# Performance work log

Measured on AMD Instinct MI355X. Metric: run time of the kernel, lower is better.

The kernel has to match this reference:

```python
import jax, jax.numpy as jnp
import numpy as np
from jax import lax

K = 2000      # node_num of GraphConvolution
H, W = 75, 100  # edge_region_feature spatial grid (from per-pixel concat loops)


def setup_inputs() -> dict:
    key = jax.random.key(0)
    k1, k2, k3, k4 = jax.random.split(key, 4)
    b, c = 8, 512
    edge_region_feature = jax.random.normal(k1, (b, c, H, W), dtype=jnp.float32)
    edge_region_predict = jax.random.normal(k2, (b, 3, H, W), dtype=jnp.float32)
    # GraphConvolution params: kaiming_normal_(fan_out) weights, zero bias
    w1 = jax.random.normal(k3, (512, 128), dtype=jnp.float32) * np.sqrt(2.0 / 128)
    b1 = jnp.zeros((K, 128), dtype=jnp.float32)
    w2 = jax.random.normal(k4, (128, 128), dtype=jnp.float32) * np.sqrt(2.0 / 128)
    b2 = jnp.zeros((K, 128), dtype=jnp.float32)
    return {"edge_region_feature": edge_region_feature,
            "edge_region_predict": edge_region_predict,
            "w1": w1, "b1": b1, "w2": w2, "b2": b2}


def reference(edge_region_feature, edge_region_predict, w1, b1, w2, b2):
    b, c = edge_region_feature.shape[0], edge_region_feature.shape[1]
    # block_feature built as: for x in range(W) for y in range(H) -> node n at (y=n%H, x=n//H)
    block = jnp.transpose(edge_region_feature, (0, 3, 2, 1)).reshape(b, W * H, c)  # (b, 7500, 512)

    # topk over channel-0 prediction, flattened row-major (idx = y*W + x)
    scores = edge_region_predict[:, 0, :, :].reshape(b, -1)            # (b, 7500)
    _vals, topk_idx = lax.top_k(scores, K)
    sorted_idx = jnp.sort(topk_idx, axis=1)                            # (b, 2000) int32

    # gather node features (replicates original's indexing of block_feature)
    node_map = jnp.take_along_axis(block, sorted_idx[:, :, None], axis=1)  # (b, 2000, 512)

    # generate_adjacent_map: decode positions with width=W, connect 8-neighborhood (+self)
    py = sorted_idx // W
    px = sorted_idx % W
    near_y = jnp.abs(py[:, :, None] - py[:, None, :]) <= 1
    near_x = jnp.abs(px[:, :, None] - px[:, None, :]) <= 1
    adj = (near_y & near_x).astype(jnp.float32)                        # (b, 2000, 2000)

    # node_feature_grouping = ReLU6 -> GCN(512->128) -> GCN(128->128)
    inp = jnp.clip(jnp.concatenate([adj, node_map], axis=2), 0.0, 6.0)  # ReLU6 on cat(adj, nodes)
    a = inp[:, :, :K]
    nf = inp[:, :, K:]
    # GCN1: A @ X @ W1 + b1  (in!=out -> no residual)
    x1 = jnp.einsum('bij,bjf->bif', a, nf) @ w1 + b1                   # (b, 2000, 128)
    # GCN2: A @ X1 @ W2 + b2 + X1 (in==out -> residual)
    x2 = jnp.einsum('bij,bjf->bif', a, x1) @ w2 + b2 + x1              # (b, 2000, 128)

    node_output_feature = jnp.tanh(x2)
    return node_output_feature, sorted_idx
```

## Files before the change

kernel.cpp:

```cpp
#include <hip/hip_runtime.h>
#include <cmath>

#define H_DIM 75
#define W_DIM 100
#define HW 7500
#define KSEL 2000
#define BATCH 8
#define CIN 512
#define FDIM 128

typedef short v4s __attribute__((ext_vector_type(4)));
typedef short v8s __attribute__((ext_vector_type(8)));
typedef float v16f __attribute__((ext_vector_type(16)));

__device__ __forceinline__ unsigned int map_key(float f) {
  unsigned int u = __float_as_uint(f);
  return (u & 0x80000000u) ? ~u : (u | 0x80000000u);
}

__device__ __forceinline__ float fast_tanh(float x) {
  float e = __expf(2.0f * x);
  return 1.0f - 2.0f * __builtin_amdgcn_rcpf(e + 1.0f);
}

__device__ __forceinline__ unsigned short bf16_rne(float v) {
  unsigned int u = __float_as_uint(v);
  unsigned int r = u + 0x7FFFu + ((u >> 16) & 1u);
  return (unsigned short)(r >> 16);
}
__device__ __forceinline__ float bf16_to_f(unsigned short h) {
  return __uint_as_float(((unsigned int)h) << 16);
}

__global__ __launch_bounds__(1024) void topk_nbr_kernel(
    const float* __restrict__ pred, const float* __restrict__ w1,
    const float* __restrict__ w2,
    int* __restrict__ off_ws, float* __restrict__ out_idx,
    unsigned short* __restrict__ nbr, unsigned char* __restrict__ cnt,
    unsigned short* __restrict__ w1t_hi, unsigned short* __restrict__ w1t_lo,
    unsigned short* __restrict__ w2t_hi, unsigned short* __restrict__ w2t_lo)
{
  __shared__ unsigned int keys[HW];
  __shared__ unsigned int whist[16 * 256];
  __shared__ unsigned int hist[256];
  __shared__ unsigned int partials[16];
  __shared__ unsigned int s_prefix, s_kth;
  const int tid = threadIdx.x;

  if (blockIdx.x >= BATCH) {
    int base = (blockIdx.x - BATCH) * 1024 + tid;
    for (int e = base; e < CIN * FDIM + FDIM * FDIM; e += 8 * 1024) {
      if (e < CIN * FDIM) {
        int k = e & (CIN - 1), f = e >> 9;
        float v = w1[k * FDIM + f];
        unsigned short hi = bf16_rne(v);
        unsigned short lo = bf16_rne(v - bf16_to_f(hi));
        w1t_hi[(size_t)f * CIN + k] = hi;
        w1t_lo[(size_t)f * CIN + k] = lo;
      } else {
        int e2 = e - CIN * FDIM;
        int k = e2 & (FDIM - 1), f = e2 >> 7;
        float v = w2[k * FDIM + f];
        unsigned short hi = bf16_rne(v);
        unsigned short lo = bf16_rne(v - bf16_to_f(hi));
        w2t_hi[(size_t)f * FDIM + k] = hi;
        w2t_lo[(size_t)f * FDIM + k] = lo;
      }
    }
    return;
  }

  const int b = blockIdx.x;
  const int lane = tid & 63, w = tid >> 6;
  const float* scores = pred + (size_t)b * 3 * HW;
  for (int i = tid; i < HW; i += 1024) keys[i] = map_key(scores[i]);
  if (tid == 0) { s_prefix = 0u; s_kth = KSEL; }
  __syncthreads();

  for (int shift = 24; shift >= 0; shift -= 8) {
    for (int i = tid; i < 16 * 256; i += 1024) whist[i] = 0u;
    __syncthreads();
    unsigned int pref = s_prefix;
    unsigned int maskhi = (shift == 24) ? 0u : (0xFFFFFFFFu << (shift + 8));
    for (int i = tid; i < HW; i += 1024) {
      unsigned int k = keys[i];
      if ((k & maskhi) == pref)
        atomicAdd(&whist[w * 256 + ((k >> shift) & 0xFFu)], 1u);
    }
    __syncthreads();
    if (tid < 256) {
      unsigned int s = 0;
      #pragma unroll
      for (int ww = 0; ww < 16; ++ww) s += whist[ww * 256 + tid];
      hist[tid] = s;
    }
    __syncthreads();
    if (tid < 64) {
      unsigned int b0 = hist[tid * 4], b1 = hist[tid * 4 + 1];
      unsigned int b2 = hist[tid * 4 + 2], b3 = hist[tid * 4 + 3];
      unsigned int kth = s_kth;
      unsigned int T = b0 + b1 + b2 + b3;
      #pragma unroll
      for (int off = 1; off < 64; off <<= 1) {
        unsigned int t = __shfl_down(T, off, 64);
        if (tid + off < 64) T += t;
      }
      unsigned int U = __shfl_down(T, 1, 64);
      if (tid == 63) U = 0u;
      unsigned int s3 = b3 + U, s2 = b2 + s3, s1 = b1 + s2, s0 = b0 + s1;
      if (s0 >= kth && s1 < kth) { s_prefix = pref | ((unsigned)(4 * tid + 0) << shift); s_kth = kth - s1; }
      if (s1 >= kth && s2 < kth) { s_prefix = pref | ((unsigned)(4 * tid + 1) << shift); s_kth = kth - s2; }
      if (s2 >= kth && s3 < kth) { s_prefix = pref | ((unsigned)(4 * tid + 2) << shift); s_kth = kth - s3; }
      if (s3 >= kth && U  < kth) { s_prefix = pref | ((unsigned)(4 * tid + 3) << shift); s_kth = kth - U; }
    }
    __syncthreads();
  }
  const unsigned int thresh = s_prefix;

  unsigned int local[8];
  unsigned int sum = 0;
  #pragma unroll
  for (int e = 0; e < 8; ++e) {
    int i = tid * 8 + e;
    unsigned int p = 0;
    if (i < HW) {
      unsigned int ky = keys[i];
      if (ky > thresh) p = 1u;
      else if (ky == thresh) p = (1u << 16);
    }
    local[e] = p; sum += p;
  }
  __syncthreads();
  short* pos_of  = (short*)keys;
  int*   s_idx_sh = (int*)((char*)keys + 15000);
  for (int i = tid; i < HW; i += 1024) pos_of[i] = -1;

  unsigned int inc = sum;
  #pragma unroll
  for (int off = 1; off < 64; off <<= 1) {
    unsigned int t = __shfl_up(inc, off, 64);
    if (lane >= off) inc += t;
  }
  if (lane == 63) partials[w] = inc;
  __syncthreads();
  if (tid < 16) {
    unsigned int v = partials[tid];
    #pragma unroll
    for (int off = 1; off < 16; off <<= 1) {
      unsigned int t = __shfl_up(v, off, 64);
      if (tid >= off) v += t;
    }
    partials[tid] = v;
  }
  __syncthreads();
  unsigned int total = partials[15];
  unsigned int run = (w ? partials[w - 1] : 0u) + inc - sum;
  unsigned int ties = (unsigned int)KSEL - (total & 0xFFFFu);
  #pragma unroll
  for (int e = 0; e < 8; ++e) {
    int i = tid * 8 + e;
    unsigned int p = local[e];
    unsigned int gt_pref = run & 0xFFFFu;
    unsigned int eq_pref = run >> 16;
    bool sel = (p & 1u) || (((p >> 16) != 0u) && eq_pref < ties);
    if (sel) {
      unsigned int pos = gt_pref + (eq_pref < ties ? eq_pref : ties);
      off_ws[b * KSEL + pos] = (i % H_DIM) * W_DIM + i / H_DIM;
      out_idx[b * KSEL + pos] = (float)i;
      s_idx_sh[pos] = i;
      pos_of[i] = (short)pos;
    }
    run += p;
  }
  __syncthreads();

  for (int i = tid; i < KSEL; i += 1024) {
    int q = s_idx_sh[i];
    int py = q / W_DIM, px = q % W_DIM;
    unsigned short tmp[9];
    int c = 0;
    #pragma unroll
    for (int dy = -1; dy <= 1; ++dy) {
      int y = py + dy;
      if ((unsigned)y >= (unsigned)H_DIM) continue;
      #pragma unroll
      for (int dx = -1; dx <= 1; ++dx) {
        int x = px + dx;
        if ((unsigned)x >= (unsigned)W_DIM) continue;
        short p = pos_of[y * W_DIM + x];
        if (p >= 0) tmp[c++] = (unsigned short)p;
      }
    }
    #pragma unroll
    for (int t = 0; t < 9; ++t)
      nbr[(size_t)(b * KSEL + i) * 9 + t] = (t < c) ? tmp[t] : (unsigned short)0;
    cnt[b * KSEL + i] = (unsigned char)c;
  }
}

__global__ __launch_bounds__(256) void gemm1_fused(
    const float* __restrict__ feat, const int* __restrict__ off_ws,
    const unsigned short* __restrict__ w1t_hi,
    const unsigned short* __restrict__ w1t_lo,
    float* __restrict__ G)
{
  __shared__ unsigned short a_hi[2][64][20], a_lo[2][64][20];
  const int b = blockIdx.y;
  const int n0 = blockIdx.x * 64;
  const int tid = threadIdx.x;
  const int lane = tid & 63, w = tid >> 6;
  const int wr = w & 1, wc = w >> 1;
  const int q = lane >> 5, m = lane & 31;
  v16f acc0, acc1;
  #pragma unroll
  for (int i = 0; i < 16; ++i) { acc0[i] = 0.f; acc1[i] = 0.f; }
  const int an = wr * 32 + m;
  const int f0 = wc * 64 + m;
  const int n_st = tid & 63, ks = (tid >> 6) * 4;
  int nidx = n0 + n_st;
  if (nidx > KSEL - 1) nidx = KSEL - 1;
  const float* fb = feat + (size_t)b * CIN * HW + off_ws[b * KSEL + nidx];

  #pragma unroll
  for (int j = 0; j < 4; ++j) {
    float v = fb[(size_t)(ks + j) * HW];
    v = fminf(fmaxf(v, 0.f), 6.f);
    unsigned short hi = bf16_rne(v);
    a_hi[0][n_st][ks + j] = hi;
    a_lo[0][n_st][ks + j] = bf16_rne(v - bf16_to_f(hi));
  }
  __syncthreads();

  for (int k0 = 0; k0 < CIN; k0 += 16) {
    const int p = (k0 >> 4) & 1;
    if (k0 + 16 < CIN) {
      #pragma unroll
      for (int j = 0; j < 4; ++j) {
        float v = fb[(size_t)(k0 + 16 + ks + j) * HW];
        v = fminf(fmaxf(v, 0.f), 6.f);
        unsigned short hi = bf16_rne(v);
        a_hi[p ^ 1][n_st][ks + j] = hi;
        a_lo[p ^ 1][n_st][ks + j] = bf16_rne(v - bf16_to_f(hi));
      }
    }
    v4s ah0 = *(const v4s*)&a_hi[p][an][q * 8];
    v4s ah1 = *(const v4s*)&a_hi[p][an][q * 8 + 4];
    v4s al0 = *(const v4s*)&a_lo[p][an][q * 8];
    v4s al1 = *(const v4s*)&a_lo[p][an][q * 8 + 4];
    v8s avh = __builtin_shufflevector(ah0, ah1, 0, 1, 2, 3, 4, 5, 6, 7);
    v8s avl = __builtin_shufflevector(al0, al1, 0, 1, 2, 3, 4, 5, 6, 7);
    v8s b0h = *(const v8s*)&w1t_hi[(size_t)f0 * CIN + k0 + q * 8];
    v8s b0l = *(const v8s*)&w1t_lo[(size_t)f0 * CIN + k0 + q * 8];
    v8s b1h = *(const v8s*)&w1t_hi[(size_t)(f0 + 32) * CIN + k0 + q * 8];
    v8s b1l = *(const v8s*)&w1t_lo[(size_t)(f0 + 32) * CIN + k0 + q * 8];
    acc0 = __builtin_amdgcn_mfma_f32_32x32x16_bf16(avh, b0h, acc0, 0, 0, 0);
    acc0 = __builtin_amdgcn_mfma_f32_32x32x16_bf16(avh, b0l, acc0, 0, 0, 0);
    acc0 = __builtin_amdgcn_mfma_f32_32x32x16_bf16(avl, b0h, acc0, 0, 0, 0);
    acc1 = __builtin_amdgcn_mfma_f32_32x32x16_bf16(avh, b1h, acc1, 0, 0, 0);
    acc1 = __builtin_amdgcn_mfma_f32_32x32x16_bf16(avh, b1l, acc1, 0, 0, 0);
    acc1 = __builtin_amdgcn_mfma_f32_32x32x16_bf16(avl, b1h, acc1, 0, 0, 0);
    __syncthreads();
  }
  float* ob = G + (size_t)b * KSEL * FDIM;
  #pragma unroll
  for (int reg = 0; reg < 16; ++reg) {
    int row = n0 + wr * 32 + (reg & 3) + 8 * (reg >> 2) + 4 * q;
    if (row < KSEL) {
      ob[(size_t)row * FDIM + f0]      = acc0[reg];
      ob[(size_t)row * FDIM + f0 + 32] = acc1[reg];
    }
  }
}

__global__ __launch_bounds__(256) void gemm2_fused(
    const float* __restrict__ G, const float* __restrict__ b1,
    const unsigned short* __restrict__ nbr, const unsigned char* __restrict__ cnt,
    const unsigned short* __restrict__ w2t_hi,
    const unsigned short* __restrict__ w2t_lo,
    float* __restrict__ x1, float* __restrict__ Hm)
{
  __shared__ __align__(16) unsigned short xh[64][FDIM];
  __shared__ __align__(16) unsigned short xl[64][FDIM];
  const int b = blockIdx.y;
  const int n0 = blockIdx.x * 64;
  const int tid = threadIdx.x;
  const int g = tid >> 5, lane32 = tid & 31;
  const float4* G4 = (const float4*)G + (size_t)b * KSEL * 32;

  #pragma unroll 2
  for (int rr = 0; rr < 8; ++rr) {
    const int r = rr * 8 + g;
    const int node = n0 + r;
    const int nodec = (node > KSEL - 1) ? KSEL - 1 : node;
    const size_t bi = (size_t)b * KSEL + nodec;
    const unsigned short* nb = nbr + bi * 9;
    unsigned short idx[9];
    #pragma unroll
    for (int t = 0; t < 9; ++t) idx[t] = nb[t];
    const int c = cnt[bi];
    float4 v[9];
    #pragma unroll
    for (int t = 0; t < 9; ++t) v[t] = G4[(size_t)idx[t] * 32 + lane32];
    float4 acc = ((const float4*)b1)[nodec * 32 + lane32];
    #pragma unroll
    for (int t = 0; t < 9; ++t) {
      float mk = (t < c) ? 1.f : 0.f;
      acc.x = fmaf(v[t].x, mk, acc.x);
      acc.y = fmaf(v[t].y, mk, acc.y);
      acc.z = fmaf(v[t].z, mk, acc.z);
      acc.w = fmaf(v[t].w, mk, acc.w);
    }
    if (node < KSEL) ((float4*)x1)[bi * 32 + lane32] = acc;
    ushort4 h, l;
    h.x = bf16_rne(acc.x); l.x = bf16_rne(acc.x - bf16_to_f(h.x));
    h.y = bf16_rne(acc.y); l.y = bf16_rne(acc.y - bf16_to_f(h.y));
    h.z = bf16_rne(acc.z); l.z = bf16_rne(acc.z - bf16_to_f(h.z));
    h.w = bf16_rne(acc.w); l.w = bf16_rne(acc.w - bf16_to_f(h.w));
    const int cs = (lane32 * 4) ^ ((r & 15) << 3);
    *(ushort4*)&xh[r][cs] = h;
    *(ushort4*)&xl[r][cs] = l;
  }
  __syncthreads();

  const int lane = tid & 63, w = tid >> 6;
  const int wr = w & 1, wc = w >> 1;
  const int q = lane >> 5, m = lane & 31;
  const int ar = wr * 32 + m;
  const int f0 = wc * 64 + m;
  v16f acc0, acc1;
  #pragma unroll
  for (int i = 0; i < 16; ++i) { acc0[i] = 0.f; acc1[i] = 0.f; }
  #pragma unroll
  for (int k0 = 0; k0 < FDIM; k0 += 16) {
    const int ac = (k0 + q * 8) ^ ((ar & 15) << 3);
    v8s avh = *(const v8s*)&xh[ar][ac];
    v8s avl = *(const v8s*)&xl[ar][ac];
    v8s b0h = *(const v8s*)&w2t_hi[(size_t)f0 * FDIM + k0 + q * 8];
    v8s b0l = *(const v8s*)&w2t_lo[(size_t)f0 * FDIM + k0 + q * 8];
    v8s b1h = *(const v8s*)&w2t_hi[(size_t)(f0 + 32) * FDIM + k0 + q * 8];
    v8s b1l = *(const v8s*)&w2t_lo[(size_t)(f0 + 32) * FDIM + k0 + q * 8];
    acc0 = __builtin_amdgcn_mfma_f32_32x32x16_bf16(avh, b0h, acc0, 0, 0, 0);
    acc0 = __builtin_amdgcn_mfma_f32_32x32x16_bf16(avh, b0l, acc0, 0, 0, 0);
    acc0 = __builtin_amdgcn_mfma_f32_32x32x16_bf16(avl, b0h, acc0, 0, 0, 0);
    acc1 = __builtin_amdgcn_mfma_f32_32x32x16_bf16(avh, b1h, acc1, 0, 0, 0);
    acc1 = __builtin_amdgcn_mfma_f32_32x32x16_bf16(avh, b1l, acc1, 0, 0, 0);
    acc1 = __builtin_amdgcn_mfma_f32_32x32x16_bf16(avl, b1h, acc1, 0, 0, 0);
  }
  float* ob = Hm + (size_t)b * KSEL * FDIM;
  #pragma unroll
  for (int reg = 0; reg < 16; ++reg) {
    int row = n0 + wr * 32 + (reg & 3) + 8 * (reg >> 2) + 4 * q;
    if (row < KSEL) {
      ob[(size_t)row * FDIM + f0]      = acc0[reg];
      ob[(size_t)row * FDIM + f0 + 32] = acc1[reg];
    }
  }
}

__global__ __launch_bounds__(256) void out_kernel(
    const float* __restrict__ Hm, const float* __restrict__ x1,
    const float* __restrict__ b2,
    const unsigned short* __restrict__ nbr, const unsigned char* __restrict__ cnt,
    float* __restrict__ out)
{
  const int g = threadIdx.x >> 5, lane = threadIdx.x & 31;
  const int node = blockIdx.x * 8 + g;
  const int bb = blockIdx.y;
  const size_t bi = (size_t)bb * KSEL + node;
  const unsigned short* nb = nbr + bi * 9;
  unsigned short idx[9];
  #pragma unroll
  for (int t = 0; t < 9; ++t) idx[t] = nb[t];
  const int c = cnt[bi];
  const float4* H4 = (const float4*)Hm + (size_t)bb * KSEL * 32;
  float4 v[9];
  #pragma unroll
  for (int t = 0; t < 9; ++t) v[t] = H4[(size_t)idx[t] * 32 + lane];
  float4 acc = ((const float4*)b2)[node * 32 + lane];
  float4 xv = ((const float4*)x1)[bi * 32 + lane];
  acc.x += xv.x; acc.y += xv.y; acc.z += xv.z; acc.w += xv.w;
  #pragma unroll
  for (int t = 0; t < 9; ++t) {
    float mk = (t < c) ? 1.f : 0.f;
    acc.x = fmaf(v[t].x, mk, acc.x);
    acc.y = fmaf(v[t].y, mk, acc.y);
    acc.z = fmaf(v[t].z, mk, acc.z);
    acc.w = fmaf(v[t].w, mk, acc.w);
  }
  float4 r;
  r.x = fast_tanh(acc.x); r.y = fast_tanh(acc.y);
  r.z = fast_tanh(acc.z); r.w = fast_tanh(acc.w);
  ((float4*)out)[bi * 32 + lane] = r;
}

extern "C" void kernel_launch(void* const* d_in, const int* in_sizes, int n_in,
                              void* d_out, int out_size, void* d_ws, size_t ws_size,
                              hipStream_t stream) {
  const float* feat = (const float*)d_in[0];
  const float* pred = (const float*)d_in[1];
  const float* w1   = (const float*)d_in[2];
  const float* b1   = (const float*)d_in[3];
  const float* w2   = (const float*)d_in[4];
  const float* b2   = (const float*)d_in[5];
  float* out0 = (float*)d_out;
  float* out_idx = out0 + (size_t)BATCH * KSEL * FDIM;

  char* ws = (char*)d_ws;
  int*            off_ws = (int*)(ws + 0);
  unsigned short* nbr    = (unsigned short*)(ws + 64256);
  unsigned char*  cnt    = (unsigned char*)(ws + 352512);
  float*          G      = (float*)(ws + 368640);
  float*          x1     = (float*)(ws + 8560640);
  float*          Hm     = (float*)(ws + 16752640);
  unsigned short* w1t_hi = (unsigned short*)(ws + 24944896);
  unsigned short* w1t_lo = (unsigned short*)(ws + 25075968);
  unsigned short* w2t_hi = (unsigned short*)(ws + 25207040);
  unsigned short* w2t_lo = (unsigned short*)(ws + 25239808);

  topk_nbr_kernel<<<BATCH + 8, 1024, 0, stream>>>(
      pred, w1, w2, off_ws, out_idx, nbr, cnt, w1t_hi, w1t_lo, w2t_hi, w2t_lo);
  gemm1_fused<<<dim3(32, BATCH), 256, 0, stream>>>(feat, off_ws, w1t_hi, w1t_lo, G);
  gemm2_fused<<<dim3(32, BATCH), 256, 0, stream>>>(G, b1, nbr, cnt, w2t_hi, w2t_lo, x1, Hm);
  out_kernel<<<dim3(KSEL / 8, BATCH), 256, 0, stream>>>(Hm, x1, b2, nbr, cnt, out0);
}
```

Baseline: 282.2 us.

## Reorder gathered nodes by row to coalesce feature gather, scatter results back

After top-k selection, the selected nodes are bucket-sorted by their feature-map row (i % H) with a shared-memory counting sort. gemm1 then gathers features in that order, so adjacent threads read nearby addresses in the (C, H, W) feature tensor. A permutation array is written out so gemm1 can scatter each output row back to its original sorted-index position. The goal is better coalescing of the strided gather, which should dominate gemm1. The cost is an extra serial prefix scan in topk, an extra int load per output row, and non-contiguous output stores.

```diff
diff --git a/kernel.cpp b/kernel.cpp
--- a/kernel.cpp
+++ b/kernel.cpp
@@ -35,7 +35,8 @@
 __global__ __launch_bounds__(1024) void topk_nbr_kernel(
     const float* __restrict__ pred, const float* __restrict__ w1,
     const float* __restrict__ w2,
-    int* __restrict__ off_ws, float* __restrict__ out_idx,
+    int* __restrict__ off2_ws, int* __restrict__ perm_ws,
+    float* __restrict__ out_idx,
     unsigned short* __restrict__ nbr, unsigned char* __restrict__ cnt,
     unsigned short* __restrict__ w1t_hi, unsigned short* __restrict__ w1t_lo,
     unsigned short* __restrict__ w2t_hi, unsigned short* __restrict__ w2t_lo)
@@ -165,7 +166,6 @@
     bool sel = (p & 1u) || (((p >> 16) != 0u) && eq_pref < ties);
     if (sel) {
       unsigned int pos = gt_pref + (eq_pref < ties ? eq_pref : ties);
-      off_ws[b * KSEL + pos] = (i % H_DIM) * W_DIM + i / H_DIM;
       out_idx[b * KSEL + pos] = (float)i;
       s_idx_sh[pos] = i;
       pos_of[i] = (short)pos;
@@ -173,6 +173,24 @@
     run += p;
   }
   __syncthreads();
+
+  if (tid < 128) hist[tid] = 0u;
+  __syncthreads();
+  for (int pos = tid; pos < KSEL; pos += 1024)
+    atomicAdd(&hist[s_idx_sh[pos] % H_DIM], 1u);
+  __syncthreads();
+  if (tid == 0) {
+    unsigned int run2 = 0u;
+    for (int j = 0; j < H_DIM; ++j) { unsigned int t = hist[j]; hist[j] = run2; run2 += t; }
+  }
+  __syncthreads();
+  for (int pos = tid; pos < KSEL; pos += 1024) {
+    int i = s_idx_sh[pos];
+    int y = i % H_DIM;
+    unsigned int j = atomicAdd(&hist[y], 1u);
+    off2_ws[b * KSEL + j] = (i % H_DIM) * W_DIM + i / H_DIM;
+    perm_ws[b * KSEL + j] = pos;
+  }
 
   for (int i = tid; i < KSEL; i += 1024) {
     int q = s_idx_sh[i];
@@ -199,7 +217,8 @@
 }
 
 __global__ __launch_bounds__(256) void gemm1_fused(
-    const float* __restrict__ feat, const int* __restrict__ off_ws,
+    const float* __restrict__ feat, const int* __restrict__ off2_ws,
+    const int* __restrict__ perm_ws,
     const unsigned short* __restrict__ w1t_hi,
     const unsigned short* __restrict__ w1t_lo,
     float* __restrict__ G)
@@ -219,7 +238,7 @@
   const int n_st = tid & 63, ks = (tid >> 6) * 4;
   int nidx = n0 + n_st;
   if (nidx > KSEL - 1) nidx = KSEL - 1;
-  const float* fb = feat + (size_t)b * CIN * HW + off_ws[b * KSEL + nidx];
+  const float* fb = feat + (size_t)b * CIN * HW + off2_ws[b * KSEL + nidx];
 
   #pragma unroll
   for (int j = 0; j < 4; ++j) {
@@ -262,12 +281,14 @@
     __syncthreads();
   }
   float* ob = G + (size_t)b * KSEL * FDIM;
+  const int* pb = perm_ws + b * KSEL;
   #pragma unroll
   for (int reg = 0; reg < 16; ++reg) {
     int row = n0 + wr * 32 + (reg & 3) + 8 * (reg >> 2) + 4 * q;
     if (row < KSEL) {
-      ob[(size_t)row * FDIM + f0]      = acc0[reg];
-      ob[(size_t)row * FDIM + f0 + 32] = acc1[reg];
+      int pr = pb[row];
+      ob[(size_t)pr * FDIM + f0]      = acc0[reg];
+      ob[(size_t)pr * FDIM + f0 + 32] = acc1[reg];
     }
   }
 }
@@ -406,20 +427,23 @@
   float* out_idx = out0 + (size_t)BATCH * KSEL * FDIM;
 
   char* ws = (char*)d_ws;
-  int*            off_ws = (int*)(ws + 0);
-  unsigned short* nbr    = (unsigned short*)(ws + 64256);
-  unsigned char*  cnt    = (unsigned char*)(ws + 352512);
-  float*          G      = (float*)(ws + 368640);
-  float*          x1     = (float*)(ws + 8560640);
-  float*          Hm     = (float*)(ws + 16752640);
-  unsigned short* w1t_hi = (unsigned short*)(ws + 24944896);
-  unsigned short* w1t_lo = (unsigned short*)(ws + 25075968);
-  unsigned short* w2t_hi = (unsigned short*)(ws + 25207040);
-  unsigned short* w2t_lo = (unsigned short*)(ws + 25239808);
+  int*            off2_ws = (int*)(ws + 0);
+  int*            perm_ws = (int*)(ws + 64256);
+  unsigned short* nbr     = (unsigned short*)(ws + 128512);
+  unsigned char*  cnt     = (unsigned char*)(ws + 416512);
+  float*          G       = (float*)(ws + 432640);
+  float*          x1      = (float*)(ws + 8624640);
+  float*          Hm      = (float*)(ws + 16816640);
+  unsigned short* w1t_hi  = (unsigned short*)(ws + 25008640);
+  unsigned short* w1t_lo  = (unsigned short*)(ws + 25139712);
+  unsigned short* w2t_hi  = (unsigned short*)(ws + 25270784);
+  unsigned short* w2t_lo  = (unsigned short*)(ws + 25303552);
 
   topk_nbr_kernel<<<BATCH + 8, 1024, 0, stream>>>(
-      pred, w1, w2, off_ws, out_idx, nbr, cnt, w1t_hi, w1t_lo, w2t_hi, w2t_lo);
-  gemm1_fused<<<dim3(32, BATCH), 256, 0, stream>>>(feat, off_ws, w1t_hi, w1t_lo, G);
+      pred, w1, w2, off2_ws, perm_ws, out_idx, nbr, cnt,
+      w1t_hi, w1t_lo, w2t_hi, w2t_lo);
+  gemm1_fused<<<dim3(32, BATCH), 256, 0, stream>>>(
+      feat, off2_ws, perm_ws, w1t_hi, w1t_lo, G);
   gemm2_fused<<<dim3(32, BATCH), 256, 0, stream>>>(G, b1, nbr, cnt, w2t_hi, w2t_lo, x1, Hm);
   out_kernel<<<dim3(KSEL / 8, BATCH), 256, 0, stream>>>(Hm, x1, b2, nbr, cnt, out0);
 }
```

Result: faster. 234.5 us (-16.9%).
